# Kernel tuning notes

Measured on AMD Instinct MI355X. Metric: run time of the kernel, lower is better.

The kernel has to match this reference:

```python
import jax, jax.numpy as jnp
import numpy as np
from functools import partial

NUM_SUPPIX = 256   # fixed number of superpixel labels (0..255)
NUM_NEIGHBORS = 9  # PatchCore-style reweighting neighbors


def euclidean_dist(x, y):
    # x: (..., N, C), y: (..., M, C) -> (..., N, M); matches torch clamp_min(0).sqrt_()
    x_norm = jnp.sum(x * x, axis=-1, keepdims=True)
    y_norm = jnp.sum(y * y, axis=-1, keepdims=True)
    res = x_norm - 2.0 * jnp.matmul(x, jnp.swapaxes(y, -2, -1)) + jnp.swapaxes(y_norm, -2, -1)
    return jnp.sqrt(jnp.clip(res, 0.0, None))


def setup_inputs() -> dict:
    key = jax.random.key(0)
    k1, k2, k3 = jax.random.split(key, 3)
    features = jax.random.normal(k1, (8, 384, 224, 224), dtype=jnp.float32)
    superpixels = jax.random.randint(k2, (8, 224, 224), 0, NUM_SUPPIX, dtype=jnp.int32)
    memory_bank = jax.random.normal(k3, (65536, 384), dtype=jnp.float32)
    return {"features": features, "superpixels": superpixels, "memory_bank": memory_bank}


def reference(features, superpixels, memory_bank):
    B, C, H, W = features.shape
    S = NUM_SUPPIX
    K = NUM_NEIGHBORS
    M = memory_bank.shape[0]

    feats = features.reshape(B, C, H * W)          # (B, C, HW)
    labels = superpixels.reshape(B, H * W)         # (B, HW)

    # --- superpixel segment-mean pooling (vectorized segment reduce) ---
    seg_sum = jax.vmap(lambda f, l: jax.ops.segment_sum(f.T, l, num_segments=S))(feats, labels)  # (B,S,C)
    counts = jax.vmap(lambda l: jax.ops.segment_sum(jnp.ones_like(l, dtype=feats.dtype), l, num_segments=S))(labels)  # (B,S)
    emb = seg_sum / jnp.maximum(counts, 1.0)[..., None]  # (B, S, C)

    # --- stage 1: nearest neighbor in memory bank ---
    emb_flat = emb.reshape(B * S, C)
    dists = euclidean_dist(emb_flat, memory_bank)        # (B*S, M)
    scores = jnp.min(dists, axis=1).reshape(B, S)        # (B, S)
    locs = jnp.argmin(dists, axis=1).reshape(B, S)       # (B, S)

    # --- stage 2: PatchCore anomaly score reweighting ---
    bidx = jnp.arange(B)
    max_patches = jnp.argmax(scores, axis=1)             # (B,)
    max_feat = emb[bidx, max_patches]                    # (B, C)
    score = scores[bidx, max_patches]                    # (B,)
    nn_index = locs[bidx, max_patches]                   # (B,)
    nn_sample = memory_bank[nn_index]                    # (B, C)

    d_nn = euclidean_dist(nn_sample, memory_bank)        # (B, M)
    _, support = jax.lax.top_k(-d_nn, min(K, M))         # smallest-K indices (B, K)
    support_feats = memory_bank[support]                 # (B, K, C)
    d_sup = euclidean_dist(max_feat[:, None, :], support_feats)[:, 0, :]  # (B, K)
    weights = (1.0 - jax.nn.softmax(d_sup, axis=1))[:, 0]
    pred_score = weights * score                         # (B,)

    # --- scatter superpixel scores back to pixel anomaly map ---
    anomaly_map = jnp.take_along_axis(scores, labels, axis=1).reshape(B, H, W)
    return anomaly_map, pred_score
```

## Files before the change

### kernel.cpp

```cpp
#include <hip/hip_runtime.h>

#define BB 8
#define CC 384
#define HWP 50176
#define SS 256
#define MM 65536
#define TOPK 9
#define GM 2048
#define NKC 16
#define RFB 2048

typedef __attribute__((ext_vector_type(8))) __bf16 bf16x8;
typedef __attribute__((ext_vector_type(16))) float fx16;
typedef __attribute__((ext_vector_type(4))) float f32x4;

__device__ __forceinline__ unsigned short f2bf_rne(float x) {
    unsigned u = __float_as_uint(x);
    unsigned r = (u + 0x7FFFu + ((u >> 16) & 1u)) >> 16;
    return (unsigned short)r;
}

__device__ __forceinline__ bf16x8 pack8(float4 v0, float4 v1) {
    bf16x8 r;
    r[0] = (__bf16)v0.x; r[1] = (__bf16)v0.y; r[2] = (__bf16)v0.z; r[3] = (__bf16)v0.w;
    r[4] = (__bf16)v1.x; r[5] = (__bf16)v1.y; r[6] = (__bf16)v1.z; r[7] = (__bf16)v1.w;
    return r;
}

__device__ __forceinline__ void gl_lds16(const void* g, void* l) {
    auto gp = (const __attribute__((address_space(1))) unsigned int*)g;
    auto lp = (__attribute__((address_space(3))) unsigned int*)l;
    __builtin_amdgcn_global_load_lds(gp, lp, 16, 0, 0);
}

__global__ void k_counts3(const int* __restrict__ labels, unsigned* __restrict__ cntS) {
    __shared__ unsigned cnt[SS];
    int kc = blockIdx.x, b = blockIdx.y;
    int t = threadIdx.x;
    cnt[t] = 0u;
    __syncthreads();
    int4 lv = ((const int4*)(labels + (size_t)b * HWP + kc * 1024))[t];
    atomicAdd(&cnt[lv.x], 1u);
    atomicAdd(&cnt[lv.y], 1u);
    atomicAdd(&cnt[lv.z], 1u);
    atomicAdd(&cnt[lv.w], 1u);
    __syncthreads();
    cntS[(kc * BB + b) * SS + t] = cnt[t];
}

template <bool ATOMIC>
__global__ __launch_bounds__(256) void k_segsum7(const float* __restrict__ feats,
                                                 const int* __restrict__ labels,
                                                 float* __restrict__ outp) {
    __shared__ bf16x8 Fs[8][64];
    __shared__ int labL[64];
    int kc = blockIdx.x, cg = blockIdx.y, b = blockIdx.z;
    int t = threadIdx.x, l = t & 63, w = t >> 6;
    int c0b = cg * 64;
    int g16 = l >> 4;
    int rowl = l & 15;

    f32x4 acc[4][4];
#pragma unroll
    for (int i = 0; i < 4; i++)
#pragma unroll
        for (int j = 0; j < 4; j++) acc[i][j] = (f32x4){0.f, 0.f, 0.f, 0.f};

    const float* fb = feats + ((size_t)b * CC + c0b) * HWP;
    const int* lbase = labels + (size_t)b * HWP + kc * 3136;

    int id0 = t * 2;
    int cl = id0 >> 3, g0 = id0 & 7;
    const float* tbase = fb + (size_t)cl * HWP + kc * 3136 + g0 * 8;

    float4 ra0 = *(const float4*)(tbase + 0);
    float4 ra1 = *(const float4*)(tbase + 4);
    float4 rb0 = *(const float4*)(tbase + 8);
    float4 rb1 = *(const float4*)(tbase + 12);
    int4 rl4 = (t < 16) ? ((const int4*)lbase)[t] : (int4){0, 0, 0, 0};

    for (int tt = 0; tt < 49; tt++) {
        __syncthreads();
        if (t < 16) ((int4*)labL)[t] = rl4;
        Fs[g0][cl] = pack8(ra0, ra1);
        Fs[g0 + 1][cl] = pack8(rb0, rb1);
        if (tt + 1 < 49) {
            const float* nb_ = tbase + (size_t)(tt + 1) * 64;
            ra0 = *(const float4*)(nb_ + 0);
            ra1 = *(const float4*)(nb_ + 4);
            rb0 = *(const float4*)(nb_ + 8);
            rb1 = *(const float4*)(nb_ + 12);
            if (t < 16) rl4 = ((const int4*)(lbase + (tt + 1) * 64))[t];
        }
        __syncthreads();

        bf16x8 af0[4], af1[4];
#pragma unroll
        for (int rt = 0; rt < 4; rt++) {
            af0[rt] = Fs[g16][rt * 16 + rowl];
            af1[rt] = Fs[4 + g16][rt * 16 + rowl];
        }
        int4 lo0 = ((int4*)labL)[g16 * 2 + 0];
        int4 hi0 = ((int4*)labL)[g16 * 2 + 1];
        int4 lo1 = ((int4*)labL)[8 + g16 * 2 + 0];
        int4 hi1 = ((int4*)labL)[8 + g16 * 2 + 1];

#pragma unroll
        for (int st = 0; st < 4; st++) {
            int tgt = w * 64 + st * 16 + rowl;
            union { unsigned u[4]; bf16x8 v; } B;
            B.u[0] = (lo0.x == tgt ? 0x3F80u : 0u) | (lo0.y == tgt ? 0x3F800000u : 0u);
            B.u[1] = (lo0.z == tgt ? 0x3F80u : 0u) | (lo0.w == tgt ? 0x3F800000u : 0u);
            B.u[2] = (hi0.x == tgt ? 0x3F80u : 0u) | (hi0.y == tgt ? 0x3F800000u : 0u);
            B.u[3] = (hi0.z == tgt ? 0x3F80u : 0u) | (hi0.w == tgt ? 0x3F800000u : 0u);
#pragma unroll
            for (int rt = 0; rt < 4; rt++)
                acc[rt][st] = __builtin_amdgcn_mfma_f32_16x16x32_bf16(af0[rt], B.v, acc[rt][st], 0, 0, 0);
            B.u[0] = (lo1.x == tgt ? 0x3F80u : 0u) | (lo1.y == tgt ? 0x3F800000u : 0u);
            B.u[1] = (lo1.z == tgt ? 0x3F80u : 0u) | (lo1.w == tgt ? 0x3F800000u : 0u);
            B.u[2] = (hi1.x == tgt ? 0x3F80u : 0u) | (hi1.y == tgt ? 0x3F800000u : 0u);
            B.u[3] = (hi1.z == tgt ? 0x3F80u : 0u) | (hi1.w == tgt ? 0x3F800000u : 0u);
#pragma unroll
            for (int rt = 0; rt < 4; rt++)
                acc[rt][st] = __builtin_amdgcn_mfma_f32_16x16x32_bf16(af1[rt], B.v, acc[rt][st], 0, 0, 0);
        }
    }

    if (ATOMIC) {
#pragma unroll
        for (int rt = 0; rt < 4; rt++)
#pragma unroll
            for (int st = 0; st < 4; st++)
#pragma unroll
                for (int r = 0; r < 4; r++) {
                    int s = w * 64 + st * 16 + rowl;
                    int c = c0b + rt * 16 + g16 * 4 + r;
                    atomicAdd(&outp[((size_t)b * SS + s) * CC + c], acc[rt][st][r]);
                }
    } else {
        float* dst = outp + (size_t)(kc * BB + b) * SS * CC;
#pragma unroll
        for (int rt = 0; rt < 4; rt++)
#pragma unroll
            for (int st = 0; st < 4; st++)
#pragma unroll
                for (int r = 0; r < 4; r++) {
                    int s = w * 64 + st * 16 + rowl;
                    int c = c0b + rt * 16 + g16 * 4 + r;
                    dst[(size_t)s * CC + c] = acc[rt][st][r];
                }
    }
}

__global__ __launch_bounds__(256) void k_cvtmb2(const float* __restrict__ mb,
                                                unsigned short* __restrict__ mbh,
                                                float* __restrict__ yn) {
    int w = threadIdx.x >> 6, l = threadIdx.x & 63;
    int r0 = blockIdx.x * 16 + w * 4;
#pragma unroll
    for (int i = 0; i < 4; i++) {
        int row = r0 + i;
        const float4* src = (const float4*)(mb + (size_t)row * CC);
        float4 a = src[l];
        float4 b2 = {0.f, 0.f, 0.f, 0.f};
        if (l < 32) b2 = src[64 + l];
        ushort4 ua; ua.x = f2bf_rne(a.x); ua.y = f2bf_rne(a.y); ua.z = f2bf_rne(a.z); ua.w = f2bf_rne(a.w);
        ((ushort4*)(mbh + (size_t)row * CC))[l] = ua;
        if (l < 32) {
            ushort4 ub; ub.x = f2bf_rne(b2.x); ub.y = f2bf_rne(b2.y); ub.z = f2bf_rne(b2.z); ub.w = f2bf_rne(b2.w);
            ((ushort4*)(mbh + (size_t)row * CC))[64 + l] = ub;
        }
        float s = a.x * a.x + a.y * a.y + a.z * a.z + a.w * a.w
                + b2.x * b2.x + b2.y * b2.y + b2.z * b2.z + b2.w * b2.w;
#pragma unroll
        for (int m = 32; m; m >>= 1) s += __shfl_xor(s, m);
        if (l == 0) yn[row] = s;
    }
}

__global__ __launch_bounds__(256) void k_ynorm2(const float* __restrict__ mb, float* __restrict__ yn) {
    int w = threadIdx.x >> 6, l = threadIdx.x & 63;
    int r0 = blockIdx.x * 16 + w * 4;
#pragma unroll
    for (int i = 0; i < 4; i++) {
        int row = r0 + i;
        const float4* src = (const float4*)(mb + (size_t)row * CC);
        float4 a = src[l];
        float4 b2 = {0.f, 0.f, 0.f, 0.f};
        if (l < 32) b2 = src[64 + l];
        float s = a.x * a.x + a.y * a.y + a.z * a.z + a.w * a.w
                + b2.x * b2.x + b2.y * b2.y + b2.z * b2.z + b2.w * b2.w;
#pragma unroll
        for (int m = 32; m; m >>= 1) s += __shfl_xor(s, m);
        if (l == 0) yn[row] = s;
    }
}

__global__ __launch_bounds__(256) void k_embfin3(const float* __restrict__ kcpart,
                                                 const unsigned* __restrict__ cntS,
                                                 float* __restrict__ emb, float* __restrict__ xn,
                                                 unsigned short* __restrict__ embh) {
    int w = threadIdx.x >> 6, l = threadIdx.x & 63;
    int i = blockIdx.x * 4 + w;
    int b = i >> 8, s256 = i & 255;
    float4 a0 = {0.f, 0.f, 0.f, 0.f}, a1 = {0.f, 0.f, 0.f, 0.f};
#pragma unroll 4
    for (int kc = 0; kc < NKC; kc++) {
        const float4* row = (const float4*)(kcpart + ((size_t)(kc * BB + b) * SS + s256) * CC);
        float4 v = row[l];
        a0.x += v.x; a0.y += v.y; a0.z += v.z; a0.w += v.w;
        if (l < 32) {
            float4 v1 = row[64 + l];
            a1.x += v1.x; a1.y += v1.y; a1.z += v1.z; a1.w += v1.w;
        }
    }
    float cw = (l < 49) ? (float)cntS[(l * BB + b) * SS + s256] : 0.f;
#pragma unroll
    for (int m = 32; m; m >>= 1) cw += __shfl_xor(cw, m);
    float inv = 1.f / fmaxf(cw, 1.f);

    a0.x *= inv; a0.y *= inv; a0.z *= inv; a0.w *= inv;
    a1.x *= inv; a1.y *= inv; a1.z *= inv; a1.w *= inv;
    ((float4*)(emb + (size_t)i * CC))[l] = a0;
    ushort4 u0; u0.x = f2bf_rne(a0.x); u0.y = f2bf_rne(a0.y); u0.z = f2bf_rne(a0.z); u0.w = f2bf_rne(a0.w);
    ((ushort4*)(embh + (size_t)i * CC))[l] = u0;
    if (l < 32) {
        ((float4*)(emb + (size_t)i * CC))[64 + l] = a1;
        ushort4 u1; u1.x = f2bf_rne(a1.x); u1.y = f2bf_rne(a1.y); u1.z = f2bf_rne(a1.z); u1.w = f2bf_rne(a1.w);
        ((ushort4*)(embh + (size_t)i * CC))[64 + l] = u1;
    }
    float ss = a0.x * a0.x + a0.y * a0.y + a0.z * a0.z + a0.w * a0.w
             + a1.x * a1.x + a1.y * a1.y + a1.z * a1.z + a1.w * a1.w;
#pragma unroll
    for (int m = 32; m; m >>= 1) ss += __shfl_xor(ss, m);
    if (l == 0) xn[i] = ss;
}

__global__ __launch_bounds__(256) void k_embfin_lm(float* __restrict__ emb,
                                                   const unsigned* __restrict__ cntS,
                                                   float* __restrict__ xn,
                                                   unsigned short* __restrict__ embh) {
    int w = threadIdx.x >> 6, l = threadIdx.x & 63;
    int i = blockIdx.x * 4 + w;
    int b = i >> 8, s256 = i & 255;
    float4* e4 = (float4*)(emb + (size_t)i * CC);
    float4 a0 = e4[l];
    float4 a1 = {0.f, 0.f, 0.f, 0.f};
    if (l < 32) a1 = e4[64 + l];
    float cw = (l < 49) ? (float)cntS[(l * BB + b) * SS + s256] : 0.f;
#pragma unroll
    for (int m = 32; m; m >>= 1) cw += __shfl_xor(cw, m);
    float inv = 1.f / fmaxf(cw, 1.f);
    a0.x *= inv; a0.y *= inv; a0.z *= inv; a0.w *= inv;
    a1.x *= inv; a1.y *= inv; a1.z *= inv; a1.w *= inv;
    e4[l] = a0;
    ushort4 u0; u0.x = f2bf_rne(a0.x); u0.y = f2bf_rne(a0.y); u0.z = f2bf_rne(a0.z); u0.w = f2bf_rne(a0.w);
    ((ushort4*)(embh + (size_t)i * CC))[l] = u0;
    if (l < 32) {
        e4[64 + l] = a1;
        ushort4 u1; u1.x = f2bf_rne(a1.x); u1.y = f2bf_rne(a1.y); u1.z = f2bf_rne(a1.z); u1.w = f2bf_rne(a1.w);
        ((ushort4*)(embh + (size_t)i * CC))[64 + l] = u1;
    }
    float ss = a0.x * a0.x + a0.y * a0.y + a0.z * a0.z + a0.w * a0.w
             + a1.x * a1.x + a1.y * a1.y + a1.z * a1.z + a1.w * a1.w;
#pragma unroll
    for (int m = 32; m; m >>= 1) ss += __shfl_xor(ss, m);
    if (l == 0) xn[i] = ss;
}

template <bool REGB>
__global__ __launch_bounds__(256) void k_gemm(
        const unsigned short* __restrict__ Ah, const unsigned short* __restrict__ Bh,
        const float* __restrict__ Bf,
        const float* __restrict__ xn, const float* __restrict__ yn,
        unsigned* __restrict__ partials) {
    __shared__ bf16x8 As[8][128];
    __shared__ bf16x8 Bs[8][128];
    __shared__ unsigned rowbest[128];
    int bid = blockIdx.x;
    int swz = (bid & 7) * 1024 + (bid >> 3);
    int rb = swz & 15, nb = swz >> 4;
    int t = threadIdx.x;
    int w = t >> 6, l = t & 63;
    int wm = w & 1, wn = w >> 1;

    if (t < 128) rowbest[t] = 0xFFFFFFFFu;

    fx16 acc00, acc01, acc10, acc11;
#pragma unroll
    for (int p = 0; p < 16; p++) { acc00[p] = 0.f; acc01[p] = 0.f; acc10[p] = 0.f; acc11[p] = 0.f; }

    const unsigned short* Abase = Ah + (size_t)(rb * 128) * CC;
    const unsigned short* Bbase = REGB ? nullptr : (Bh + (size_t)(nb * 128) * CC);
    const float* Bfbase = Bf + (size_t)(nb * 128) * CC;

    for (int kt = 0; kt < 6; kt++) {
        int k0 = kt * 64;
#pragma unroll
        for (int q = 0; q < 4; q++) {
            int c = q * 256 + t;
            int r = c & 127, g = c >> 7;
            gl_lds16(Abase + (size_t)r * CC + k0 + g * 8, &As[g][r]);
            if (!REGB) {
                gl_lds16(Bbase + (size_t)r * CC + k0 + g * 8, &Bs[g][r]);
            } else {
                const float* src = Bfbase + (size_t)r * CC + k0 + g * 8;
                float4 v0 = *(const float4*)(src);
                float4 v1 = *(const float4*)(src + 4);
                Bs[g][r] = pack8(v0, v1);
            }
        }
        __syncthreads();
#pragma unroll
        for (int s = 0; s < 4; s++) {
            int g = s * 2 + (l >> 5);
            bf16x8 a0 = As[g][wm * 64 + (l & 31)];
            bf16x8 a1 = As[g][wm * 64 + 32 + (l & 31)];
            bf16x8 b0 = Bs[g][wn * 64 + (l & 31)];
            bf16x8 b1 = Bs[g][wn * 64 + 32 + (l & 31)];
            acc00 = __builtin_amdgcn_mfma_f32_32x32x16_bf16(a0, b0, acc00, 0, 0, 0);
            acc01 = __builtin_amdgcn_mfma_f32_32x32x16_bf16(a0, b1, acc01, 0, 0, 0);
            acc10 = __builtin_amdgcn_mfma_f32_32x32x16_bf16(a1, b0, acc10, 0, 0, 0);
            acc11 = __builtin_amdgcn_mfma_f32_32x32x16_bf16(a1, b1, acc11, 0, 0, 0);
        }
        __syncthreads();
    }

    int coll0 = wn * 64 + (l & 31);
    int coll1 = coll0 + 32;
    float yn0 = yn[nb * 128 + coll0], yn1 = yn[nb * 128 + coll1];
#pragma unroll
    for (int i = 0; i < 2; i++) {
#pragma unroll
        for (int p = 0; p < 16; p++) {
            float a0v = (i == 0) ? acc00[p] : acc10[p];
            float a1v = (i == 0) ? acc01[p] : acc11[p];
            int rl = i * 32 + (p & 3) + 8 * (p >> 2) + 4 * (l >> 5);
            float xr = xn[rb * 128 + wm * 64 + rl];
            float d0 = fmaxf(xr - 2.f * a0v + yn0, 0.f);
            float d1 = fmaxf(xr - 2.f * a1v + yn1, 0.f);
            unsigned k0 = (__float_as_uint(d0) & 0xFFFFFF00u) | (unsigned)coll0;
            unsigned k1 = (__float_as_uint(d1) & 0xFFFFFF00u) | (unsigned)coll1;
            unsigned best = k0 < k1 ? k0 : k1;
#pragma unroll
            for (int m = 1; m < 32; m <<= 1) {
                unsigned o2 = __shfl_xor(best, m);
                if (o2 < best) best = o2;
            }
            if ((l & 31) == 0) atomicMin(&rowbest[wm * 64 + rl], best);
        }
    }
    __syncthreads();
    if (t < 128) partials[(size_t)nb * GM + rb * 128 + t] = rowbest[t];
}

__global__ void k_reduce1(const unsigned* __restrict__ partials,
                          unsigned long long* __restrict__ partial2) {
    int row = blockIdx.x * 256 + threadIdx.x;
    int ng = blockIdx.y;
    unsigned long long m = ~0ull;
    for (int n = 0; n < 64; n++) {
        int nb = ng * 64 + n;
        unsigned k = partials[(size_t)nb * GM + row];
        unsigned long long v = ((unsigned long long)(k & 0xFFFFFF00u) << 32)
                             | (unsigned)(nb * 128 + (k & 0xFFu));
        if (v < m) m = v;
    }
    partial2[ng * GM + row] = m;
}

__global__ void k_reduce2cand(const unsigned long long* __restrict__ partial2,
                              float* __restrict__ scores, int* __restrict__ locs,
                              int* __restrict__ cand) {
    __shared__ unsigned long long key[256];
    __shared__ unsigned long long red[256];
    int b = blockIdx.x, t = threadIdx.x;
    int row = b * 256 + t;
    unsigned long long m = ~0ull;
    for (int g = 0; g < 8; g++) {
        unsigned long long v = partial2[g * GM + row];
        if (v < m) m = v;
    }
    float sc = sqrtf(__uint_as_float((unsigned)(m >> 32)));
    scores[row] = sc;
    locs[row] = (int)(m & 0xffffffffu);
    key[t] = ((unsigned long long)__float_as_uint(sc) << 32) | (unsigned)(255 - t);
    __syncthreads();
    for (int k = 0; k < 4; k++) {
        red[t] = key[t];
        __syncthreads();
        for (int s = 128; s; s >>= 1) {
            if (t < s && red[t + s] > red[t]) red[t] = red[t + s];
            __syncthreads();
        }
        unsigned long long win = red[0];
        int patch = 255 - (int)(win & 0xffffffffu);
        if (t == 0) cand[b * 4 + k] = b * SS + patch;
        __syncthreads();
        if (t == patch) key[t] = 0;
        __syncthreads();
    }
}

__global__ __launch_bounds__(256) void k_refine2(
        const float* __restrict__ emb, const float* __restrict__ mb,
        const float* __restrict__ xn, const float* __restrict__ yn,
        const int* __restrict__ cand, unsigned long long* __restrict__ refpart) {
    __shared__ float cl[32 * CC];
    __shared__ float xnc[32];
    __shared__ int cr[32];
    __shared__ unsigned long long wbest[4][32];
    int t = threadIdx.x, w = t >> 6, l = t & 63;
    if (t < 32) cr[t] = cand[t];
    __syncthreads();
    if (t < 32) xnc[t] = xn[cr[t]];
    for (int i = t; i < 32 * CC; i += 256) {
        int j = i / CC, p = i - j * CC;
        cl[i] = emb[(size_t)cr[j] * CC + p];
    }
    __syncthreads();

    unsigned long long best = ~0ull;
#pragma unroll
    for (int g = 0; g < 4; g++) {
        int m0 = blockIdx.x * 32 + g * 8 + w * 2, m1 = m0 + 1;
        float2 r0[3], r1[3];
#pragma unroll
        for (int c = 0; c < 3; c++) {
            r0[c] = *(const float2*)&mb[(size_t)m0 * CC + c * 128 + l * 2];
            r1[c] = *(const float2*)&mb[(size_t)m1 * CC + c * 128 + l * 2];
        }
        float ya = yn[m0], yb = yn[m1];
#pragma unroll 2
        for (int j = 0; j < 32; j++) {
            float s0 = 0.f, s1 = 0.f;
#pragma unroll
            for (int c = 0; c < 3; c++) {
                float2 cv = *(const float2*)&cl[j * CC + c * 128 + l * 2];
                s0 = fmaf(r0[c].x, cv.x, s0); s0 = fmaf(r0[c].y, cv.y, s0);
                s1 = fmaf(r1[c].x, cv.x, s1); s1 = fmaf(r1[c].y, cv.y, s1);
            }
#pragma unroll
            for (int mm = 32; mm; mm >>= 1) { s0 += __shfl_xor(s0, mm); s1 += __shfl_xor(s1, mm); }
            float d0 = fmaxf(xnc[j] - 2.f * s0 + ya, 0.f);
            float d1 = fmaxf(xnc[j] - 2.f * s1 + yb, 0.f);
            unsigned long long k0 = ((unsigned long long)__float_as_uint(d0) << 32) | (unsigned)m0;
            unsigned long long k1 = ((unsigned long long)__float_as_uint(d1) << 32) | (unsigned)m1;
            unsigned long long kb = k0 < k1 ? k0 : k1;
            if (l == j && kb < best) best = kb;
        }
    }
    if (l < 32) wbest[w][l] = best;
    __syncthreads();
    if (t < 32) {
        unsigned long long m = wbest[0][t];
        if (wbest[1][t] < m) m = wbest[1][t];
        if (wbest[2][t] < m) m = wbest[2][t];
        if (wbest[3][t] < m) m = wbest[3][t];
        refpart[(size_t)blockIdx.x * 32 + t] = m;
    }
}

__global__ void k_refred(const unsigned long long* __restrict__ refpart,
                         unsigned long long* __restrict__ keys2) {
    __shared__ unsigned long long red[256];
    int j = blockIdx.x, t = threadIdx.x;
    unsigned long long m = ~0ull;
    for (int i = t; i < RFB; i += 256) {
        unsigned long long v = refpart[(size_t)i * 32 + j];
        if (v < m) m = v;
    }
    red[t] = m;
    __syncthreads();
    for (int s = 128; s; s >>= 1) {
        if (t < s && red[t + s] < red[t]) red[t] = red[t + s];
        __syncthreads();
    }
    if (t == 0) keys2[j] = red[0];
}

__global__ void k_final(const unsigned long long* __restrict__ keys2, const int* __restrict__ cand,
                        int* __restrict__ mp, float* __restrict__ scb, int* __restrict__ nn) {
    int b = threadIdx.x;
    if (b < BB) {
        float bestsc = -1.f;
        int bestpatch = 1 << 20, bestnn = 0;
        for (int k = 0; k < 4; k++) {
            unsigned long long key = keys2[b * 4 + k];
            float sc = sqrtf(__uint_as_float((unsigned)(key >> 32)));
            int patch = cand[b * 4 + k] & 255;
            int nnidx = (int)(key & 0xffffffffu);
            if (sc > bestsc || (sc == bestsc && patch < bestpatch)) {
                bestsc = sc; bestpatch = patch; bestnn = nnidx;
            }
        }
        mp[b] = bestpatch; scb[b] = bestsc; nn[b] = bestnn;
    }
}

__global__ __launch_bounds__(256) void k_dnn2(const float* __restrict__ mb,
                                              const float* __restrict__ yn,
                                              const int* __restrict__ nn,
                                              float* __restrict__ dnn) {
    __shared__ float nnf[BB][CC];
    __shared__ float ynn[BB];
    int t = threadIdx.x, w = t >> 6, l = t & 63;
    for (int i = t; i < BB * CC; i += 256) {
        int bb = i / CC, cc = i - bb * CC;
        nnf[bb][cc] = mb[(size_t)nn[bb] * CC + cc];
    }
    if (t < BB) ynn[t] = yn[nn[t]];
    __syncthreads();
#pragma unroll
    for (int i = 0; i < 4; i++) {
        int m = blockIdx.x * 16 + w * 4 + i;
        const float4* r4 = (const float4*)(mb + (size_t)m * CC);
        float4 va = r4[l];
        float4 vb = {0.f, 0.f, 0.f, 0.f};
        if (l < 32) vb = r4[64 + l];
        float ym = yn[m];
#pragma unroll
        for (int b = 0; b < BB; b++) {
            const float4* n4 = (const float4*)nnf[b];
            float4 na = n4[l];
            float s = va.x * na.x + va.y * na.y + va.z * na.z + va.w * na.w;
            if (l < 32) {
                float4 nb2 = n4[64 + l];
                s += vb.x * nb2.x + vb.y * nb2.y + vb.z * nb2.z + vb.w * nb2.w;
            }
#pragma unroll
            for (int mm = 32; mm; mm >>= 1) s += __shfl_xor(s, mm);
            if (l == 0) {
                float d2 = fmaxf(ynn[b] - 2.f * s + ym, 0.f);
                dnn[(size_t)b * MM + m] = sqrtf(d2);
            }
        }
    }
}

__global__ void k_top9a(const float* __restrict__ dnn, float* __restrict__ t9v,
                        int* __restrict__ t9i) {
    __shared__ float sd[256][TOPK];
    __shared__ int sx[256][TOPK];
    int c = blockIdx.x, b = blockIdx.y, t = threadIdx.x;
    float ld[TOPK];
    int li[TOPK];
#pragma unroll
    for (int k = 0; k < TOPK; k++) { ld[k] = INFINITY; li[k] = MM; }
    const float* d = dnn + (size_t)b * MM;
    for (int m = c * 1024 + t; m < (c + 1) * 1024; m += 256) {
        float v = d[m];
        if (v < ld[TOPK - 1] || (v == ld[TOPK - 1] && m < li[TOPK - 1])) {
            int k = TOPK - 1;
            while (k > 0 && (v < ld[k - 1] || (v == ld[k - 1] && m < li[k - 1]))) {
                ld[k] = ld[k - 1]; li[k] = li[k - 1]; k--;
            }
            ld[k] = v; li[k] = m;
        }
    }
    for (int k = 0; k < TOPK; k++) { sd[t][k] = ld[k]; sx[t][k] = li[k]; }
    __syncthreads();
    for (int s = 128; s; s >>= 1) {
        if (t < s) {
            float md[TOPK]; int mi[TOPK];
            int p = 0, q = 0;
            for (int k = 0; k < TOPK; k++) {
                float va = sd[t][p], vb = sd[t + s][q];
                int ia = sx[t][p], ib = sx[t + s][q];
                bool ta = (va < vb) || (va == vb && ia < ib);
                if (ta) { md[k] = va; mi[k] = ia; p++; }
                else    { md[k] = vb; mi[k] = ib; q++; }
            }
            for (int k = 0; k < TOPK; k++) { sd[t][k] = md[k]; sx[t][k] = mi[k]; }
        }
        __syncthreads();
    }
    if (t < TOPK) {
        t9v[(b * 64 + c) * TOPK + t] = sd[0][t];
        t9i[(b * 64 + c) * TOPK + t] = sx[0][t];
    }
}

__global__ void k_fintop(const float* __restrict__ t9v, const int* __restrict__ t9i,
                         const float* __restrict__ emb, const float* __restrict__ mb,
                         const float* __restrict__ yn, const float* __restrict__ xn,
                         const int* __restrict__ mp, const float* __restrict__ scb,
                         float* __restrict__ outp) {
    __shared__ float sd[256][TOPK];
    __shared__ int sx[256][TOPK];
    __shared__ int supl[TOPK];
    __shared__ float ds[TOPK];
    int b = blockIdx.x, t = threadIdx.x;
    float ld[TOPK];
    int li[TOPK];
#pragma unroll
    for (int k = 0; k < TOPK; k++) { ld[k] = INFINITY; li[k] = MM; }
    for (int i = t; i < 64 * TOPK; i += 256) {
        float v = t9v[b * 64 * TOPK + i];
        int m = t9i[b * 64 * TOPK + i];
        if (v < ld[TOPK - 1] || (v == ld[TOPK - 1] && m < li[TOPK - 1])) {
            int k = TOPK - 1;
            while (k > 0 && (v < ld[k - 1] || (v == ld[k - 1] && m < li[k - 1]))) {
                ld[k] = ld[k - 1]; li[k] = li[k - 1]; k--;
            }
            ld[k] = v; li[k] = m;
        }
    }
    for (int k = 0; k < TOPK; k++) { sd[t][k] = ld[k]; sx[t][k] = li[k]; }
    __syncthreads();
    for (int s = 128; s; s >>= 1) {
        if (t < s) {
            float md[TOPK]; int mi[TOPK];
            int p = 0, q = 0;
            for (int k = 0; k < TOPK; k++) {
                float va = sd[t][p], vb = sd[t + s][q];
                int ia = sx[t][p], ib = sx[t + s][q];
                bool ta = (va < vb) || (va == vb && ia < ib);
                if (ta) { md[k] = va; mi[k] = ia; p++; }
                else    { md[k] = vb; mi[k] = ib; q++; }
            }
            for (int k = 0; k < TOPK; k++) { sd[t][k] = md[k]; sx[t][k] = mi[k]; }
        }
        __syncthreads();
    }
    if (t < TOPK) supl[t] = sx[0][t];
    __syncthreads();

    int w = t >> 6, l = t & 63;
    int mpb = mp[b];
    const float* mf = emb + ((size_t)b * SS + mpb) * CC;
    float xr = xn[b * SS + mpb];
    for (int k = w; k < TOPK; k += 4) {
        int sidx = supl[k];
        const float* sr = mb + (size_t)sidx * CC;
        float s = 0.f;
#pragma unroll
        for (int i = 0; i < 6; i++) s = fmaf(mf[i * 64 + l], sr[i * 64 + l], s);
#pragma unroll
        for (int mm = 32; mm; mm >>= 1) s += __shfl_xor(s, mm);
        if (l == 0) ds[k] = sqrtf(fmaxf(xr - 2.f * s + yn[sidx], 0.f));
    }
    __syncthreads();
    if (t == 0) {
        float mx = ds[0];
        for (int k = 1; k < TOPK; k++) mx = fmaxf(mx, ds[k]);
        float num = expf(ds[0] - mx), den = 0.f;
        for (int k = 0; k < TOPK; k++) den += expf(ds[k] - mx);
        outp[b] = (1.f - num / den) * scb[b];
    }
}

__global__ void k_map4(const float* __restrict__ scores, const int* __restrict__ labels,
                       float* __restrict__ out) {
    size_t i4 = (size_t)blockIdx.x * 256 + threadIdx.x;
    int b = (int)(i4 / (HWP / 4));
    int4 lv = ((const int4*)labels)[i4];
    const float* sb = scores + b * SS;
    float4 o;
    o.x = sb[lv.x]; o.y = sb[lv.y]; o.z = sb[lv.z]; o.w = sb[lv.w];
    ((float4*)out)[i4] = o;
}

extern "C" void kernel_launch(void* const* d_in, const int* in_sizes, int n_in,
                              void* d_out, int out_size, void* d_ws, size_t ws_size,
                              hipStream_t stream) {
    const float* feats  = (const float*)d_in[0];
    const int*   labels = (const int*)d_in[1];
    const float* mb     = (const float*)d_in[2];
    float* out = (float*)d_out;

    char* ws = (char*)d_ws;
    const size_t SZ_MBH   = (size_t)MM * CC * 2;
    const size_t SZ_EMBH  = (size_t)GM * CC * 2;
    const size_t SZ_EMB   = (size_t)GM * CC * 4;
    const size_t SZ_YN    = (size_t)MM * 4;
    const size_t SZ_SMALL = 8192;
    const size_t SZ_CNTS  = (size_t)49 * BB * SS * 4;
    const size_t SZ_P2    = (size_t)8 * GM * 8;
    const size_t SZ_T9    = (size_t)BB * 64 * TOPK * 4;
    const size_t SZ_KCP   = (size_t)NKC * BB * SS * CC * 4;
    const size_t SZ_BIG   = SZ_KCP;

    size_t need_full = SZ_MBH + SZ_EMBH + SZ_EMB + SZ_YN + 3 * SZ_SMALL + SZ_CNTS + 2048
                     + SZ_P2 + 2 * SZ_T9 + SZ_BIG + 1024;
    bool lowmem = ws_size < need_full;

    size_t o = 0;
    unsigned short* mbh = nullptr;
    if (!lowmem) { mbh = (unsigned short*)(ws + o); o += SZ_MBH; }
    unsigned short* embh = (unsigned short*)(ws + o); o += SZ_EMBH;
    float* emb = (float*)(ws + o);                    o += SZ_EMB;
    float* yn  = (float*)(ws + o);                    o += SZ_YN;
    float* xn  = (float*)(ws + o);                    o += SZ_SMALL;
    float* scores = (float*)(ws + o);                 o += SZ_SMALL;
    int*   locs   = (int*)(ws + o);                   o += SZ_SMALL;
    unsigned* cntS = (unsigned*)(ws + o);             o += SZ_CNTS;
    int*   cand   = (int*)(ws + o);                   o += 256;
    unsigned long long* keys2 = (unsigned long long*)(ws + o); o += 256;
    int*   mp  = (int*)(ws + o);                      o += 128;
    float* scb = (float*)(ws + o);                    o += 128;
    int*   nn  = (int*)(ws + o);                      o += 128;
    o = (o + 255) & ~(size_t)255;
    float* t9v = (float*)(ws + o);                    o += SZ_T9;
    int*   t9i = (int*)(ws + o);                      o += SZ_T9;
    o = (o + 255) & ~(size_t)255;
    unsigned long long* partial2 = (unsigned long long*)(ws + o); o += SZ_P2;
    char* big = ws + o;
    float* kcpart = (float*)big;
    unsigned* partials = (unsigned*)big;
    unsigned long long* refpart  = (unsigned long long*)big;
    float* dnn = (float*)(big + 4194304);

    k_counts3<<<dim3(49, BB), 256, 0, stream>>>(labels, cntS);

    if (!lowmem) {
        k_segsum7<false><<<dim3(NKC, 6, BB), 256, 0, stream>>>(feats, labels, kcpart);
        k_cvtmb2<<<MM / 16, 256, 0, stream>>>(mb, mbh, yn);
        k_embfin3<<<GM / 4, 256, 0, stream>>>(kcpart, cntS, emb, xn, embh);
        k_gemm<false><<<8192, 256, 0, stream>>>(embh, mbh, mb, xn, yn, partials);
    } else {
        hipMemsetAsync(emb, 0, SZ_EMB, stream);
        k_segsum7<true><<<dim3(NKC, 6, BB), 256, 0, stream>>>(feats, labels, emb);
        k_ynorm2<<<MM / 16, 256, 0, stream>>>(mb, yn);
        k_embfin_lm<<<GM / 4, 256, 0, stream>>>(emb, cntS, xn, embh);
        k_gemm<true><<<8192, 256, 0, stream>>>(embh, embh, mb, xn, yn, partials);
    }

    k_reduce1<<<dim3(8, 8), 256, 0, stream>>>(partials, partial2);
    k_reduce2cand<<<BB, 256, 0, stream>>>(partial2, scores, locs, cand);
    k_refine2<<<RFB, 256, 0, stream>>>(emb, mb, xn, yn, cand, refpart);
    k_refred<<<32, 256, 0, stream>>>(refpart, keys2);
    k_final<<<1, 64, 0, stream>>>(keys2, cand, mp, scb, nn);
    k_dnn2<<<MM / 16, 256, 0, stream>>>(mb, yn, nn, dnn);
    k_top9a<<<dim3(64, BB), 256, 0, stream>>>(dnn, t9v, t9i);
    k_fintop<<<BB, 256, 0, stream>>>(t9v, t9i, emb, mb, yn, xn, mp, scb, out + (size_t)BB * HWP);
    k_map4<<<(BB * HWP / 4) / 256, 256, 0, stream>>>(scores, labels, out);
}
```

Measured before the change: 681.8 us.

## Rewrite refine and dnn kernels to per-lane dot products without shuffle reductions

```diff
diff --git a/kernel.cpp b/kernel.cpp
--- a/kernel.cpp
+++ b/kernel.cpp
@@ -8,7 +8,7 @@
 #define TOPK 9
 #define GM 2048
 #define NKC 16
-#define RFB 2048
+#define RFB3 1024
 
 typedef __attribute__((ext_vector_type(8))) __bf16 bf16x8;
 typedef __attribute__((ext_vector_type(16))) float fx16;
@@ -402,61 +402,55 @@
     }
 }
 
-__global__ __launch_bounds__(256) void k_refine2(
+__global__ __launch_bounds__(256) void k_refine3(
         const float* __restrict__ emb, const float* __restrict__ mb,
         const float* __restrict__ xn, const float* __restrict__ yn,
         const int* __restrict__ cand, unsigned long long* __restrict__ refpart) {
-    __shared__ float cl[32 * CC];
+    __shared__ float clT[CC][32];
     __shared__ float xnc[32];
     __shared__ int cr[32];
-    __shared__ unsigned long long wbest[4][32];
+    __shared__ unsigned long long wbest[4][64];
     int t = threadIdx.x, w = t >> 6, l = t & 63;
     if (t < 32) cr[t] = cand[t];
     __syncthreads();
     if (t < 32) xnc[t] = xn[cr[t]];
-    for (int i = t; i < 32 * CC; i += 256) {
-        int j = i / CC, p = i - j * CC;
-        cl[i] = emb[(size_t)cr[j] * CC + p];
-    }
-    __syncthreads();
-
+    {
+        int j = t & 31;
+        int r = cr[j];
+        for (int kk = t >> 5; kk < CC; kk += 8)
+            clT[kk][j] = emb[(size_t)r * CC + kk];
+    }
+    __syncthreads();
+
+    int j = l & 31;
+    int half = l >> 5;
     unsigned long long best = ~0ull;
 #pragma unroll
-    for (int g = 0; g < 4; g++) {
-        int m0 = blockIdx.x * 32 + g * 8 + w * 2, m1 = m0 + 1;
-        float2 r0[3], r1[3];
-#pragma unroll
-        for (int c = 0; c < 3; c++) {
-            r0[c] = *(const float2*)&mb[(size_t)m0 * CC + c * 128 + l * 2];
-            r1[c] = *(const float2*)&mb[(size_t)m1 * CC + c * 128 + l * 2];
-        }
-        float ya = yn[m0], yb = yn[m1];
-#pragma unroll 2
-        for (int j = 0; j < 32; j++) {
-            float s0 = 0.f, s1 = 0.f;
-#pragma unroll
-            for (int c = 0; c < 3; c++) {
-                float2 cv = *(const float2*)&cl[j * CC + c * 128 + l * 2];
-                s0 = fmaf(r0[c].x, cv.x, s0); s0 = fmaf(r0[c].y, cv.y, s0);
-                s1 = fmaf(r1[c].x, cv.x, s1); s1 = fmaf(r1[c].y, cv.y, s1);
-            }
-#pragma unroll
-            for (int mm = 32; mm; mm >>= 1) { s0 += __shfl_xor(s0, mm); s1 += __shfl_xor(s1, mm); }
-            float d0 = fmaxf(xnc[j] - 2.f * s0 + ya, 0.f);
-            float d1 = fmaxf(xnc[j] - 2.f * s1 + yb, 0.f);
-            unsigned long long k0 = ((unsigned long long)__float_as_uint(d0) << 32) | (unsigned)m0;
-            unsigned long long k1 = ((unsigned long long)__float_as_uint(d1) << 32) | (unsigned)m1;
-            unsigned long long kb = k0 < k1 ? k0 : k1;
-            if (l == j && kb < best) best = kb;
-        }
-    }
-    if (l < 32) wbest[w][l] = best;
+    for (int pr = 0; pr < 8; pr++) {
+        int m = blockIdx.x * 64 + w * 16 + pr * 2 + half;
+        const float4* r4 = (const float4*)(mb + (size_t)m * CC);
+        float s = 0.f;
+#pragma unroll 8
+        for (int k4 = 0; k4 < CC / 4; k4++) {
+            float4 v = r4[k4];
+            s = fmaf(v.x, clT[k4 * 4 + 0][j], s);
+            s = fmaf(v.y, clT[k4 * 4 + 1][j], s);
+            s = fmaf(v.z, clT[k4 * 4 + 2][j], s);
+            s = fmaf(v.w, clT[k4 * 4 + 3][j], s);
+        }
+        float d2 = fmaxf(xnc[j] - 2.f * s + yn[m], 0.f);
+        unsigned long long key = ((unsigned long long)__float_as_uint(d2) << 32) | (unsigned)m;
+        if (key < best) best = key;
+    }
+    wbest[w][l] = best;
     __syncthreads();
     if (t < 32) {
-        unsigned long long m = wbest[0][t];
-        if (wbest[1][t] < m) m = wbest[1][t];
-        if (wbest[2][t] < m) m = wbest[2][t];
-        if (wbest[3][t] < m) m = wbest[3][t];
+        unsigned long long m = ~0ull;
+#pragma unroll
+        for (int ww = 0; ww < 4; ww++) {
+            if (wbest[ww][t] < m) m = wbest[ww][t];
+            if (wbest[ww][t + 32] < m) m = wbest[ww][t + 32];
+        }
         refpart[(size_t)blockIdx.x * 32 + t] = m;
     }
 }
@@ -466,7 +460,7 @@
     __shared__ unsigned long long red[256];
     int j = blockIdx.x, t = threadIdx.x;
     unsigned long long m = ~0ull;
-    for (int i = t; i < RFB; i += 256) {
+    for (int i = t; i < RFB3; i += 256) {
         unsigned long long v = refpart[(size_t)i * 32 + j];
         if (v < m) m = v;
     }
@@ -498,44 +492,35 @@
     }
 }
 
-__global__ __launch_bounds__(256) void k_dnn2(const float* __restrict__ mb,
+__global__ __launch_bounds__(256) void k_dnn3(const float* __restrict__ mb,
                                               const float* __restrict__ yn,
                                               const int* __restrict__ nn,
                                               float* __restrict__ dnn) {
-    __shared__ float nnf[BB][CC];
+    __shared__ float4 nnT[CC / 4][BB];
     __shared__ float ynn[BB];
     int t = threadIdx.x, w = t >> 6, l = t & 63;
-    for (int i = t; i < BB * CC; i += 256) {
-        int bb = i / CC, cc = i - bb * CC;
-        nnf[bb][cc] = mb[(size_t)nn[bb] * CC + cc];
+    for (int i = t; i < (CC / 4) * BB; i += 256) {
+        int k4 = i >> 3, b = i & 7;
+        nnT[k4][b] = ((const float4*)(mb + (size_t)nn[b] * CC))[k4];
     }
     if (t < BB) ynn[t] = yn[nn[t]];
     __syncthreads();
-#pragma unroll
-    for (int i = 0; i < 4; i++) {
-        int m = blockIdx.x * 16 + w * 4 + i;
-        const float4* r4 = (const float4*)(mb + (size_t)m * CC);
-        float4 va = r4[l];
-        float4 vb = {0.f, 0.f, 0.f, 0.f};
-        if (l < 32) vb = r4[64 + l];
-        float ym = yn[m];
-#pragma unroll
-        for (int b = 0; b < BB; b++) {
-            const float4* n4 = (const float4*)nnf[b];
-            float4 na = n4[l];
-            float s = va.x * na.x + va.y * na.y + va.z * na.z + va.w * na.w;
-            if (l < 32) {
-                float4 nb2 = n4[64 + l];
-                s += vb.x * nb2.x + vb.y * nb2.y + vb.z * nb2.z + vb.w * nb2.w;
-            }
-#pragma unroll
-            for (int mm = 32; mm; mm >>= 1) s += __shfl_xor(s, mm);
-            if (l == 0) {
-                float d2 = fmaxf(ynn[b] - 2.f * s + ym, 0.f);
-                dnn[(size_t)b * MM + m] = sqrtf(d2);
-            }
-        }
-    }
+
+    int b = l & 7, mg = l >> 3;
+    int m = blockIdx.x * 32 + w * 8 + mg;
+    const float4* r4 = (const float4*)(mb + (size_t)m * CC);
+    float s = 0.f;
+#pragma unroll 8
+    for (int k4 = 0; k4 < CC / 4; k4++) {
+        float4 v = r4[k4];
+        float4 n = nnT[k4][b];
+        s = fmaf(v.x, n.x, s);
+        s = fmaf(v.y, n.y, s);
+        s = fmaf(v.z, n.z, s);
+        s = fmaf(v.w, n.w, s);
+    }
+    float d2 = fmaxf(ynn[b] - 2.f * s + yn[m], 0.f);
+    dnn[(size_t)b * MM + m] = sqrtf(d2);
 }
 
 __global__ void k_top9a(const float* __restrict__ dnn, float* __restrict__ t9v,
@@ -728,10 +713,10 @@
 
     k_reduce1<<<dim3(8, 8), 256, 0, stream>>>(partials, partial2);
     k_reduce2cand<<<BB, 256, 0, stream>>>(partial2, scores, locs, cand);
-    k_refine2<<<RFB, 256, 0, stream>>>(emb, mb, xn, yn, cand, refpart);
+    k_refine3<<<RFB3, 256, 0, stream>>>(emb, mb, xn, yn, cand, refpart);
     k_refred<<<32, 256, 0, stream>>>(refpart, keys2);
     k_final<<<1, 64, 0, stream>>>(keys2, cand, mp, scb, nn);
-    k_dnn2<<<MM / 16, 256, 0, stream>>>(mb, yn, nn, dnn);
+    k_dnn3<<<MM / 32, 256, 0, stream>>>(mb, yn, nn, dnn);
     k_top9a<<<dim3(64, BB), 256, 0, stream>>>(dnn, t9v, t9i);
     k_fintop<<<BB, 256, 0, stream>>>(t9v, t9i, emb, mb, yn, xn, mp, scb, out + (size_t)BB * HWP);
     k_map4<<<(BB * HWP / 4) / 256, 256, 0, stream>>>(scores, labels, out);
```

Measured after the change: 613.4 us. -10.0%, faster.
